# Performance work log

Measured on AMD Instinct MI355X. Metric: run time of the kernel, lower is better.

The kernel has to match this reference:

```python
import jax, jax.numpy as jnp
import numpy as np

D = 32  # latent_dim
# relation order for stacked params: 0=ss, 1=tt, 2=st, 3=ts

def setup_inputs() -> dict:
    key = jax.random.key(0)
    ks = jax.random.split(key, 6)
    B, N, T = 32, 1024, 256
    spatial_nodes = jax.random.normal(ks[0], (B, N, D), dtype=jnp.float32)
    temporal_nodes = jax.random.normal(ks[1], (B, T, D), dtype=jnp.float32)
    # Linear(2D, 1) weights for the 4 relation MLPs and 4 mask MLPs, stacked.
    scale = 1.0 / np.sqrt(2 * D)
    W_rel = jax.random.uniform(ks[2], (4, 2 * D), jnp.float32, -scale, scale)
    b_rel = jax.random.uniform(ks[3], (4,), jnp.float32, -scale, scale)
    W_mask = jax.random.uniform(ks[4], (4, 2 * D), jnp.float32, -scale, scale)
    b_mask = jax.random.uniform(ks[5], (4,), jnp.float32, -scale, scale)
    return {"spatial_nodes": spatial_nodes, "temporal_nodes": temporal_nodes,
            "W_rel": W_rel, "b_rel": b_rel, "W_mask": W_mask, "b_mask": b_mask}


def _sub_graph(x1, x2, w_rel, brel, w_mask, bmask):
    # Linear applied to concat(x1_i, x2_j) decomposes as x1_i@w[:D] + x2_j@w[D:] + b,
    # avoiding the O(B*N1*N2*2D) concat intermediate of the original code.
    a1 = x1 @ w_rel[:D]          # [B, N1]
    a2 = x2 @ w_rel[D:]          # [B, N2]
    adj = a1[:, :, None] + a2[:, None, :] + brel   # [B, N1, N2]
    m1 = x1 @ w_mask[:D]
    m2 = x2 @ w_mask[D:]
    mask = jax.nn.relu(m1[:, :, None] + m2[:, None, :] + bmask)
    return adj, mask


def reference(spatial_nodes, temporal_nodes, W_rel, b_rel, W_mask, b_mask):
    s, t = spatial_nodes, temporal_nodes
    ss_a, ss_m = _sub_graph(s, s, W_rel[0], b_rel[0], W_mask[0], b_mask[0])
    tt_a, tt_m = _sub_graph(t, t, W_rel[1], b_rel[1], W_mask[1], b_mask[1])
    st_a, st_m = _sub_graph(s, t, W_rel[2], b_rel[2], W_mask[2], b_mask[2])
    ts_a, ts_m = _sub_graph(t, s, W_rel[3], b_rel[3], W_mask[3], b_mask[3])
    adj = jnp.concatenate([
        jnp.concatenate([ss_a, st_a], axis=-1),
        jnp.concatenate([ts_a, tt_a], axis=-1)], axis=-2)   # [B, N+T, N+T]
    mask = jnp.concatenate([
        jnp.concatenate([ss_m, st_m], axis=-1),
        jnp.concatenate([ts_m, tt_m], axis=-1)], axis=-2)
    adj = jnp.tanh(adj * mask)
    # Per-batch sparse edge extraction (nonzero/gather) in the original has
    # data-dependent shapes; it is a pure re-indexing of adj's nonzeros and is
    # omitted from the jit-compatible dense reference output.
    return adj
```

## Files before the change

### kernel.cpp

```cpp
#include <hip/hip_runtime.h>
#include <cstddef>

#define D_  32
#define N_  1024
#define T_  256
#define NT_ 1280
#define B_  32

#define RA_OFF 0
#define RM_OFF (B_*NT_*2)
#define CA_OFF (2*B_*NT_*2)
#define CM_OFF (CA_OFF + 2*B_*NT_)

#define RPB 16

__device__ __forceinline__ float fast_tanh(float x) {
    float e = __expf(2.0f * x);
    return 1.0f - 2.0f * __builtin_amdgcn_rcpf(e + 1.0f);
}

__device__ __forceinline__ float dot8(const float4* __restrict__ xv,
                                      const float* __restrict__ w) {
    const float4* wv = (const float4*)w;
    float a = 0.f;
    #pragma unroll
    for (int k = 0; k < D_ / 4; ++k) {
        float4 ww = wv[k];
        a = fmaf(xv[k].x, ww.x, a);
        a = fmaf(xv[k].y, ww.y, a);
        a = fmaf(xv[k].z, ww.z, a);
        a = fmaf(xv[k].w, ww.w, a);
    }
    return a;
}

__global__ __launch_bounds__(256) void proj_kernel(
    const float* __restrict__ S,  const float* __restrict__ Tn,
    const float* __restrict__ Wr, const float* __restrict__ br,
    const float* __restrict__ Wm, const float* __restrict__ bm,
    float* __restrict__ ws)
{
    const int idx = blockIdx.x * 256 + threadIdx.x;
    const int b   = blockIdx.y;
    const int seg = (idx >= N_);
    const float* x = seg ? (Tn + ((size_t)b * T_ + (idx - N_)) * D_)
                         : (S  + ((size_t)b * N_ +  idx      ) * D_);
    float4 xv[D_ / 4];
    #pragma unroll
    for (int k = 0; k < D_ / 4; ++k) xv[k] = ((const float4*)x)[k];

    const int rr0 = seg ? 3 : 0;
    const int rr1 = seg ? 1 : 2;
    float* RA = ws + RA_OFF;  float* RM = ws + RM_OFF;
    const size_t ri = ((size_t)b * NT_ + idx) * 2;
    float2 rav, rmv;
    rav.x = dot8(xv, Wr + rr0 * 2 * D_) + br[rr0];
    rav.y = dot8(xv, Wr + rr1 * 2 * D_) + br[rr1];
    rmv.x = dot8(xv, Wm + rr0 * 2 * D_) + bm[rr0];
    rmv.y = dot8(xv, Wm + rr1 * 2 * D_) + bm[rr1];
    *(float2*)&RA[ri] = rav;
    *(float2*)&RM[ri] = rmv;

    const int rc0 = seg ? 2 : 0;
    const int rc1 = seg ? 1 : 3;
    float* CA = ws + CA_OFF;  float* CM = ws + CM_OFF;
    const size_t ci = (size_t)b * NT_ + idx;
    CA[0 * B_ * NT_ + ci] = dot8(xv, Wr + rc0 * 2 * D_ + D_);
    CA[1 * B_ * NT_ + ci] = dot8(xv, Wr + rc1 * 2 * D_ + D_);
    CM[0 * B_ * NT_ + ci] = dot8(xv, Wm + rc0 * 2 * D_ + D_);
    CM[1 * B_ * NT_ + ci] = dot8(xv, Wm + rc1 * 2 * D_ + D_);
}

__global__ __launch_bounds__(320) void epi_kernel(
    const float* __restrict__ ws, float* __restrict__ out)
{
    const int tid   = threadIdx.x;
    const int i0    = blockIdx.x * RPB;
    const int b     = blockIdx.y;
    const int seg_i = (i0  >= N_);
    const int seg_j = (tid >= 256) ? 1 : 0;

    const float* RA = ws + RA_OFF;
    const float* RM = ws + RM_OFF;
    const float* CA = ws + CA_OFF;
    const float* CM = ws + CM_OFF;

    const int j = tid * 4;
    const size_t cbase = ((size_t)seg_i * B_ + b) * NT_ + j;
    const float4 ca = *(const float4*)&CA[cbase];
    const float4 cm = *(const float4*)&CM[cbase];

    const float2* RAp = (const float2*)&RA[((size_t)b * NT_ + i0) * 2];
    const float2* RMp = (const float2*)&RM[((size_t)b * NT_ + i0) * 2];
    float* orow = out + ((size_t)(b * NT_ + i0)) * NT_ + j;

    #pragma unroll
    for (int r = 0; r < RPB; ++r) {
        const float2 rav = RAp[r];
        const float2 rmv = RMp[r];
        const float  ra  = seg_j ? rav.y : rav.x;
        const float  rm  = seg_j ? rmv.y : rmv.x;
        float4 o;
        o.x = fast_tanh((ra + ca.x) * fmaxf(rm + cm.x, 0.f));
        o.y = fast_tanh((ra + ca.y) * fmaxf(rm + cm.y, 0.f));
        o.z = fast_tanh((ra + ca.z) * fmaxf(rm + cm.z, 0.f));
        o.w = fast_tanh((ra + ca.w) * fmaxf(rm + cm.w, 0.f));
        *(float4*)(orow + (size_t)r * NT_) = o;
    }
}

extern "C" void kernel_launch(void* const* d_in, const int* in_sizes, int n_in,
                              void* d_out, int out_size, void* d_ws, size_t ws_size,
                              hipStream_t stream) {
    const float* S  = (const float*)d_in[0];
    const float* Tn = (const float*)d_in[1];
    const float* Wr = (const float*)d_in[2];
    const float* br = (const float*)d_in[3];
    const float* Wm = (const float*)d_in[4];
    const float* bm = (const float*)d_in[5];
    float* out = (float*)d_out;
    float* ws  = (float*)d_ws;

    proj_kernel<<<dim3(NT_ / 256, B_), 256, 0, stream>>>(S, Tn, Wr, br, Wm, bm, ws);
    epi_kernel <<<dim3(NT_ / RPB, B_), 320, 0, stream>>>(ws, out);
}
```

Before: 218.4 us.

## Fuse projection and epilogue kernels, recomputing column projections per block in LDS

Merges the projection kernel into the epilogue kernel. Each block recomputes the column projections for all 1280 columns of its batch and its own row projections into shared memory, then writes the tanh outputs. This removes the second launch and the workspace round trip, but every block re-reads all node features and redoes the column dot products, adding redundant reads and compute to an output-write-bound kernel.

```diff
diff --git a/kernel.cpp b/kernel.cpp
--- a/kernel.cpp
+++ b/kernel.cpp
@@ -7,20 +7,17 @@
 #define NT_ 1280
 #define B_  32
 
-#define RA_OFF 0
-#define RM_OFF (B_*NT_*2)
-#define CA_OFF (2*B_*NT_*2)
-#define CM_OFF (CA_OFF + 2*B_*NT_)
+#define RPB 16
+#define THR 320
 
-#define RPB 16
 
 __device__ __forceinline__ float fast_tanh(float x) {
     float e = __expf(2.0f * x);
     return 1.0f - 2.0f * __builtin_amdgcn_rcpf(e + 1.0f);
 }
 
-__device__ __forceinline__ float dot8(const float4* __restrict__ xv,
-                                      const float* __restrict__ w) {
+__device__ __forceinline__ float dot32(const float4* __restrict__ xv,
+                                       const float* __restrict__ w) {
     const float4* wv = (const float4*)w;
     float a = 0.f;
     #pragma unroll
@@ -34,70 +31,64 @@
     return a;
 }
 
-__global__ __launch_bounds__(256) void proj_kernel(
+__global__ __launch_bounds__(THR) void fused_kernel(
     const float* __restrict__ S,  const float* __restrict__ Tn,
     const float* __restrict__ Wr, const float* __restrict__ br,
     const float* __restrict__ Wm, const float* __restrict__ bm,
-    float* __restrict__ ws)
+    float* __restrict__ out)
 {
-    const int idx = blockIdx.x * 256 + threadIdx.x;
-    const int b   = blockIdx.y;
-    const int seg = (idx >= N_);
-    const float* x = seg ? (Tn + ((size_t)b * T_ + (idx - N_)) * D_)
-                         : (S  + ((size_t)b * N_ +  idx      ) * D_);
-    float4 xv[D_ / 4];
-    #pragma unroll
-    for (int k = 0; k < D_ / 4; ++k) xv[k] = ((const float4*)x)[k];
+    __shared__ float  ca_s[NT_];
+    __shared__ float  cm_s[NT_];
+    __shared__ float2 ra_s[RPB];
+    __shared__ float2 rm_s[RPB];
 
-    const int rr0 = seg ? 3 : 0;
-    const int rr1 = seg ? 1 : 2;
-    float* RA = ws + RA_OFF;  float* RM = ws + RM_OFF;
-    const size_t ri = ((size_t)b * NT_ + idx) * 2;
-    float2 rav, rmv;
-    rav.x = dot8(xv, Wr + rr0 * 2 * D_) + br[rr0];
-    rav.y = dot8(xv, Wr + rr1 * 2 * D_) + br[rr1];
-    rmv.x = dot8(xv, Wm + rr0 * 2 * D_) + bm[rr0];
-    rmv.y = dot8(xv, Wm + rr1 * 2 * D_) + bm[rr1];
-    *(float2*)&RA[ri] = rav;
-    *(float2*)&RM[ri] = rmv;
-
-    const int rc0 = seg ? 2 : 0;
-    const int rc1 = seg ? 1 : 3;
-    float* CA = ws + CA_OFF;  float* CM = ws + CM_OFF;
-    const size_t ci = (size_t)b * NT_ + idx;
-    CA[0 * B_ * NT_ + ci] = dot8(xv, Wr + rc0 * 2 * D_ + D_);
-    CA[1 * B_ * NT_ + ci] = dot8(xv, Wr + rc1 * 2 * D_ + D_);
-    CM[0 * B_ * NT_ + ci] = dot8(xv, Wm + rc0 * 2 * D_ + D_);
-    CM[1 * B_ * NT_ + ci] = dot8(xv, Wm + rc1 * 2 * D_ + D_);
-}
-
-__global__ __launch_bounds__(320) void epi_kernel(
-    const float* __restrict__ ws, float* __restrict__ out)
-{
     const int tid   = threadIdx.x;
     const int i0    = blockIdx.x * RPB;
     const int b     = blockIdx.y;
-    const int seg_i = (i0  >= N_);
-    const int seg_j = (tid >= 256) ? 1 : 0;
+    const int seg_i = (i0 >= N_);
+    const int r0    = seg_i ? 3 : 0;
+    const int r1    = seg_i ? 1 : 2;
 
-    const float* RA = ws + RA_OFF;
-    const float* RM = ws + RM_OFF;
-    const float* CA = ws + CA_OFF;
-    const float* CM = ws + CM_OFF;
+    #pragma unroll
+    for (int c = 0; c < 4; ++c) {
+        const int j  = tid + c * THR;
+        const int sj = (j >= N_);
+        const float* xj = sj ? (Tn + ((size_t)b * T_ + (j - N_)) * D_)
+                             : (S  + ((size_t)b * N_ +  j      ) * D_);
+        float4 xv[D_ / 4];
+        #pragma unroll
+        for (int k = 0; k < D_ / 4; ++k) xv[k] = ((const float4*)xj)[k];
+        const int rc = sj ? r1 : r0;
+        ca_s[j] = dot32(xv, Wr + rc * 2 * D_ + D_);
+        cm_s[j] = dot32(xv, Wm + rc * 2 * D_ + D_);
+    }
 
-    const int j = tid * 4;
-    const size_t cbase = ((size_t)seg_i * B_ + b) * NT_ + j;
-    const float4 ca = *(const float4*)&CA[cbase];
-    const float4 cm = *(const float4*)&CM[cbase];
+    if (tid < RPB * 4) {
+        const int r = tid >> 2, q = tid & 3;
+        const int i = i0 + r;
+        const float* xi = seg_i ? (Tn + ((size_t)b * T_ + (i - N_)) * D_)
+                                : (S  + ((size_t)b * N_ +  i      ) * D_);
+        float4 xv[D_ / 4];
+        #pragma unroll
+        for (int k = 0; k < D_ / 4; ++k) xv[k] = ((const float4*)xi)[k];
+        const int rs = (q & 1) ? r1 : r0;
+        const float* W  = (q < 2) ? Wr : Wm;
+        const float* bb = (q < 2) ? br : bm;
+        const float v = dot32(xv, W + rs * 2 * D_) + bb[rs];
+        float* dst = (q < 2) ? (float*)ra_s : (float*)rm_s;
+        dst[r * 2 + (q & 1)] = v;
+    }
+    __syncthreads();
 
-    const float2* RAp = (const float2*)&RA[((size_t)b * NT_ + i0) * 2];
-    const float2* RMp = (const float2*)&RM[((size_t)b * NT_ + i0) * 2];
-    float* orow = out + ((size_t)(b * NT_ + i0)) * NT_ + j;
+    const int   seg_j = (tid >= 256);
+    const float4 ca = *(const float4*)&ca_s[tid * 4];
+    const float4 cm = *(const float4*)&cm_s[tid * 4];
+    float* orow = out + ((size_t)(b * NT_ + i0)) * NT_ + tid * 4;
 
     #pragma unroll
     for (int r = 0; r < RPB; ++r) {
-        const float2 rav = RAp[r];
-        const float2 rmv = RMp[r];
+        const float2 rav = ra_s[r];
+        const float2 rmv = rm_s[r];
         const float  ra  = seg_j ? rav.y : rav.x;
         const float  rm  = seg_j ? rmv.y : rmv.x;
         float4 o;
@@ -119,8 +110,6 @@
     const float* Wm = (const float*)d_in[4];
     const float* bm = (const float*)d_in[5];
     float* out = (float*)d_out;
-    float* ws  = (float*)d_ws;
 
-    proj_kernel<<<dim3(NT_ / 256, B_), 256, 0, stream>>>(S, Tn, Wr, br, Wm, bm, ws);
-    epi_kernel <<<dim3(NT_ / RPB, B_), 320, 0, stream>>>(ws, out);
+    fused_kernel<<<dim3(NT_ / RPB, B_), THR, 0, stream>>>(S, Tn, Wr, br, Wm, bm, out);
 }
```

New measurement: 265.5 us. +21.6%, slower.
